# Performance work log

Measured on AMD Instinct MI355X. Metric: run time of the kernel, lower is better.

## Reference

```python
import jax, jax.numpy as jnp
import numpy as np

DIM = 2048
NUM_HEADS = 8
HEAD_DIM = DIM // NUM_HEADS
BATCH = 16384
EPS = 1e-5


def setup_inputs() -> dict:
    key = jax.random.key(0)
    ks = jax.random.split(key, 10)
    s = 1.0 / np.sqrt(DIM)
    inp = {
        "x": jax.random.normal(ks[0], (BATCH, 1, DIM), dtype=jnp.float32),
        "w_q": jax.random.uniform(ks[1], (DIM, DIM), jnp.float32, -s, s),
        "b_q": jax.random.uniform(ks[2], (DIM,), jnp.float32, -s, s),
        "w_k": jax.random.uniform(ks[3], (DIM, DIM), jnp.float32, -s, s),
        "b_k": jax.random.uniform(ks[4], (DIM,), jnp.float32, -s, s),
        "w_v": jax.random.uniform(ks[5], (DIM, DIM), jnp.float32, -s, s),
        "b_v": jax.random.uniform(ks[6], (DIM,), jnp.float32, -s, s),
        "w_o": jax.random.uniform(ks[7], (DIM, DIM), jnp.float32, -s, s),
        "b_o": jax.random.uniform(ks[8], (DIM,), jnp.float32, -s, s),
        "ln_gamma": jnp.ones((DIM,), jnp.float32),
        "ln_beta": jnp.zeros((DIM,), jnp.float32),
    }
    return inp


def _layer_norm(x, gamma, beta):
    mean = jnp.mean(x, axis=-1, keepdims=True)
    var = jnp.mean(jnp.square(x - mean), axis=-1, keepdims=True)
    return (x - mean) * jax.lax.rsqrt(var + EPS) * gamma + beta


def reference(x, w_q, b_q, w_k, b_k, w_v, b_v, w_o, b_o, ln_gamma, ln_beta):
    # x: (B, 1, D). Dropout is identity (eval mode).
    residual = x
    h = _layer_norm(x, ln_gamma, ln_beta)
    q = h @ w_q.T + b_q  # (B, 1, D)
    k = h @ w_k.T + b_k
    v = h @ w_v.T + b_v
    B = x.shape[0]
    # (B, H, 1, hd)
    qh = q.reshape(B, 1, NUM_HEADS, HEAD_DIM).transpose(0, 2, 1, 3)
    kh = k.reshape(B, 1, NUM_HEADS, HEAD_DIM).transpose(0, 2, 1, 3)
    vh = v.reshape(B, 1, NUM_HEADS, HEAD_DIM).transpose(0, 2, 1, 3)
    scale = HEAD_DIM ** -0.5
    # (B, H, 1, 1); with seq_len=1 softmax is trivially 1, but keep the math faithful
    scores = jnp.einsum("bhqd,bhkd->bhqk", qh, kh) * scale
    probs = jax.nn.softmax(scores, axis=-1)
    attn = jnp.einsum("bhqk,bhkd->bhqd", probs, vh)  # (B, H, 1, hd)
    attn = attn.transpose(0, 2, 1, 3).reshape(B, 1, DIM)
    out = attn @ w_o.T + b_o
    out = out + residual
    return out[:, 0, :]  # squeeze seq dim -> (B, D)
```

## Files before the change

### kernel.cpp

```cpp
#include <hip/hip_runtime.h>
#include <hip/hip_bf16.h>
#include <cstdint>

#define D_MODEL 2048
#define N_BATCH 16384

typedef __attribute__((ext_vector_type(8))) __bf16 bf16x8;
typedef __attribute__((ext_vector_type(4))) float f32x4;

__device__ __forceinline__ unsigned short f2bf(float f) {
    unsigned int u = __builtin_bit_cast(unsigned int, f);
    u += 0x7fffu + ((u >> 16) & 1u);
    return (unsigned short)(u >> 16);
}

__global__ __launch_bounds__(256) void ln_kernel(
    const float* __restrict__ x, const float* __restrict__ gamma,
    const float* __restrict__ beta, unsigned short* __restrict__ h)
{
    const int row = blockIdx.x;
    const int t = threadIdx.x;
    const float4* x4 = reinterpret_cast<const float4*>(x + (long)row * D_MODEL);
    float4 a = x4[t];
    float4 b = x4[256 + t];
    float s  = a.x + a.y + a.z + a.w + b.x + b.y + b.z + b.w;
    float ss = a.x*a.x + a.y*a.y + a.z*a.z + a.w*a.w
             + b.x*b.x + b.y*b.y + b.z*b.z + b.w*b.w;
    #pragma unroll
    for (int off = 32; off; off >>= 1) {
        s  += __shfl_xor(s, off);
        ss += __shfl_xor(ss, off);
    }
    __shared__ float red[8];
    const int lane = t & 63, wid = t >> 6;
    if (lane == 0) { red[wid*2] = s; red[wid*2+1] = ss; }
    __syncthreads();
    s  = red[0] + red[2] + red[4] + red[6];
    ss = red[1] + red[3] + red[5] + red[7];
    const float mean = s * (1.0f / D_MODEL);
    const float var  = ss * (1.0f / D_MODEL) - mean * mean;
    const float inv  = rsqrtf(var + 1e-5f);

    const float4* g4  = reinterpret_cast<const float4*>(gamma);
    const float4* be4 = reinterpret_cast<const float4*>(beta);
    ushort4* h4 = reinterpret_cast<ushort4*>(h + (long)row * D_MODEL);
    {
        float4 g = g4[t], be = be4[t];
        ushort4 o;
        o.x = f2bf((a.x - mean) * inv * g.x + be.x);
        o.y = f2bf((a.y - mean) * inv * g.y + be.y);
        o.z = f2bf((a.z - mean) * inv * g.z + be.z);
        o.w = f2bf((a.w - mean) * inv * g.w + be.w);
        h4[t] = o;
    }
    {
        float4 g = g4[256 + t], be = be4[256 + t];
        ushort4 o;
        o.x = f2bf((b.x - mean) * inv * g.x + be.x);
        o.y = f2bf((b.y - mean) * inv * g.y + be.y);
        o.z = f2bf((b.z - mean) * inv * g.z + be.z);
        o.w = f2bf((b.w - mean) * inv * g.w + be.w);
        h4[256 + t] = o;
    }
}

__global__ __launch_bounds__(256) void transpose_f32_to_bf16(
    const float* __restrict__ in, unsigned short* __restrict__ out, int Dm)
{
    __shared__ float tile[32][33];
    const int nb = Dm >> 5;
    const int k0 = (blockIdx.x % nb) * 32;
    const int j0 = (blockIdx.x / nb) * 32;
    const int tx = threadIdx.x & 31, ty0 = threadIdx.x >> 5;
    #pragma unroll
    for (int i = 0; i < 32; i += 8) {
        int j = ty0 + i;
        tile[j][tx] = in[(long)(j0 + j) * Dm + k0 + tx];
    }
    __syncthreads();
    #pragma unroll
    for (int i = 0; i < 32; i += 8) {
        int kk = ty0 + i;
        out[(long)(k0 + kk) * Dm + j0 + tx] = f2bf(tile[tx][kk]);
    }
}

__global__ __launch_bounds__(256) void convert_bf16(
    const float* __restrict__ in, unsigned short* __restrict__ out, long n)
{
    long i = ((long)blockIdx.x * 256 + threadIdx.x) * 8;
    if (i >= n) return;
    const float4* in4 = reinterpret_cast<const float4*>(in + i);
    float4 a = in4[0], b = in4[1];
    union { unsigned short u[8]; uint4 v; } o;
    o.u[0] = f2bf(a.x); o.u[1] = f2bf(a.y); o.u[2] = f2bf(a.z); o.u[3] = f2bf(a.w);
    o.u[4] = f2bf(b.x); o.u[5] = f2bf(b.y); o.u[6] = f2bf(b.z); o.u[7] = f2bf(b.w);
    *reinterpret_cast<uint4*>(out + i) = o.v;
}

__global__ __launch_bounds__(256) void bias_combine(
    const float* __restrict__ w_o, const float* __restrict__ b_v,
    const float* __restrict__ b_o, float* __restrict__ b_c)
{
    const int n = blockIdx.x;
    const int t = threadIdx.x;
    const float4* w4 = reinterpret_cast<const float4*>(w_o + (long)n * D_MODEL);
    const float4* v4 = reinterpret_cast<const float4*>(b_v);
    float4 a = w4[t], b = w4[256 + t], va = v4[t], vb = v4[256 + t];
    float s = a.x*va.x + a.y*va.y + a.z*va.z + a.w*va.w
            + b.x*vb.x + b.y*vb.y + b.z*vb.z + b.w*vb.w;
    #pragma unroll
    for (int off = 32; off; off >>= 1) s += __shfl_xor(s, off);
    __shared__ float red[4];
    const int lane = t & 63, wid = t >> 6;
    if (lane == 0) red[wid] = s;
    __syncthreads();
    if (t == 0) b_c[n] = red[0] + red[1] + red[2] + red[3] + b_o[n];
}

__global__ __launch_bounds__(256, 2) void gemm_bt_128(
    const unsigned short* __restrict__ A, const unsigned short* __restrict__ B,
    unsigned short* __restrict__ C, int M, int N, int K)
{
    const int nBN = N >> 7;
    int wg = blockIdx.x;
    const int nwg = gridDim.x;
    const int cpx = nwg >> 3;
    wg = (wg & 7) * cpx + (wg >> 3);
    const int bm = wg / nBN, bn = wg % nBN;

    const int t = threadIdx.x;
    const int lane = t & 63, wid = t >> 6;
    const int wr = wid >> 1, wc = wid & 1;

    __shared__ __align__(16) unsigned short Alds[128 * 32];
    __shared__ __align__(16) unsigned short Blds[128 * 32];

    f32x4 acc[4][4];
    #pragma unroll
    for (int i = 0; i < 4; i++)
        #pragma unroll
        for (int j = 0; j < 4; j++) acc[i][j] = (f32x4){0.f, 0.f, 0.f, 0.f};

    const long Abase = (long)bm * 128 * K;
    const long Bbase = (long)bn * 128 * K;
    const int ci0 = wid * 64 + lane;
    const int ci1 = 256 + ci0;
    const int r0 = ci0 >> 2, c0 = (ci0 & 3) * 8;
    const int r1 = ci1 >> 2, c1 = (ci1 & 3) * 8;

    const int arow = wr * 64 + (lane & 15);
    const int brow = wc * 64 + (lane & 15);
    const int koff = (lane >> 4) * 8;

    for (int k0 = 0; k0 < K; k0 += 32) {
        __builtin_amdgcn_global_load_lds(
            (const __attribute__((address_space(1))) void*)(A + Abase + (long)r0 * K + k0 + c0),
            (__attribute__((address_space(3))) void*)(Alds + wid * 512), 16, 0, 0);
        __builtin_amdgcn_global_load_lds(
            (const __attribute__((address_space(1))) void*)(A + Abase + (long)r1 * K + k0 + c1),
            (__attribute__((address_space(3))) void*)(Alds + 2048 + wid * 512), 16, 0, 0);
        __builtin_amdgcn_global_load_lds(
            (const __attribute__((address_space(1))) void*)(B + Bbase + (long)r0 * K + k0 + c0),
            (__attribute__((address_space(3))) void*)(Blds + wid * 512), 16, 0, 0);
        __builtin_amdgcn_global_load_lds(
            (const __attribute__((address_space(1))) void*)(B + Bbase + (long)r1 * K + k0 + c1),
            (__attribute__((address_space(3))) void*)(Blds + 2048 + wid * 512), 16, 0, 0);
        __syncthreads();

        bf16x8 af[4], bfr[4];
        #pragma unroll
        for (int m = 0; m < 4; m++)
            af[m] = *reinterpret_cast<const bf16x8*>(&Alds[(arow + m * 16) * 32 + koff]);
        #pragma unroll
        for (int n = 0; n < 4; n++)
            bfr[n] = *reinterpret_cast<const bf16x8*>(&Blds[(brow + n * 16) * 32 + koff]);
        #pragma unroll
        for (int m = 0; m < 4; m++)
            #pragma unroll
            for (int n = 0; n < 4; n++)
                acc[m][n] = __builtin_amdgcn_mfma_f32_16x16x32_bf16(af[m], bfr[n], acc[m][n], 0, 0, 0);
        __syncthreads();
    }

    const int crow0 = bm * 128 + wr * 64 + ((lane >> 4) << 2);
    const int ccol0 = bn * 128 + wc * 64 + (lane & 15);
    #pragma unroll
    for (int m = 0; m < 4; m++)
        #pragma unroll
        for (int j = 0; j < 4; j++) {
            const long r = crow0 + m * 16 + j;
            #pragma unroll
            for (int n = 0; n < 4; n++)
                C[r * N + ccol0 + n * 16] = f2bf(acc[m][n][j]);
        }
}

#define GLL(src, dst) __builtin_amdgcn_global_load_lds( \
    (const __attribute__((address_space(1))) void*)(src), \
    (__attribute__((address_space(3))) void*)(dst), 16, 0, 0)
#define WAITV4() do { asm volatile("s_waitcnt vmcnt(4)" ::: "memory"); \
                      __builtin_amdgcn_sched_barrier(0); } while (0)
#define WAITV0() do { asm volatile("s_waitcnt vmcnt(0)" ::: "memory"); \
                      __builtin_amdgcn_sched_barrier(0); } while (0)

__global__ __launch_bounds__(512, 2) void gemm_bt_8ph(
    const unsigned short* __restrict__ A, const unsigned short* __restrict__ B,
    float* __restrict__ C, const float* __restrict__ bias,
    const float* __restrict__ resid, int M, int N, int K)
{
    __shared__ __align__(16) char ldsb[131072];

    const int nBN = N >> 8;
    int wg = blockIdx.x;
    const int cpx = gridDim.x >> 3;
    wg = (wg & 7) * cpx + (wg >> 3);
    const int bm = wg / nBN, bn = wg % nBN;

    const int t = threadIdx.x;
    const int lane = t & 63, wid = t >> 6;
    const int wr = wid >> 2;
    const int wc = wid & 3;

    const long Kl = K;
    const int tr = t >> 3;
    const int c8 = ((t & 7) ^ (tr & 7)) * 8;
    const unsigned short* As = A + (long)(bm * 256 + tr) * Kl + c8;
    const unsigned short* Bs = B + (long)(bn * 256 + tr) * Kl + c8;

#define ST_A(buf, half, kcol) do { \
    const unsigned short* s_ = As + (half) * 128 * Kl + (kcol); \
    char* d_ = ldsb + (buf) * 65536 + (half) * 16384 + t * 16; \
    GLL(s_, d_); GLL(s_ + 64 * Kl, d_ + 8192); } while (0)
#define ST_B(buf, half, kcol) do { \
    const unsigned short* s_ = Bs + (half) * 128 * Kl + (kcol); \
    char* d_ = ldsb + (buf) * 65536 + 32768 + (half) * 16384 + t * 16; \
    GLL(s_, d_); GLL(s_ + 64 * Kl, d_ + 8192); } while (0)

    const int l15 = lane & 15, l4 = lane >> 4;
    const int swz0 = ((l4)     ^ (l15 & 7)) << 4;
    const int swz1 = ((4 + l4) ^ (l15 & 7)) << 4;
    const int aOff = wr * 16384 + l15 * 128;
    const int bOff = 32768 + (wc >> 1) * 16384 + ((wc & 1) * 64 + l15) * 128;

#define LDV(off) (*reinterpret_cast<const bf16x8*>(ldsb + (off)))
#define RD_A(buf, mh) do { _Pragma("unroll") for (int mi = 0; mi < 4; ++mi) { \
    af[mi][0] = LDV((buf) * 65536 + aOff + ((mh) * 4 + mi) * 2048 + swz0); \
    af[mi][1] = LDV((buf) * 65536 + aOff + ((mh) * 4 + mi) * 2048 + swz1); } } while (0)
#define RD_B0(buf) do { _Pragma("unroll") for (int nj = 0; nj < 2; ++nj) { \
    b0[nj][0] = LDV((buf) * 65536 + bOff + nj * 2048 + swz0); \
    b0[nj][1] = LDV((buf) * 65536 + bOff + nj * 2048 + swz1); } } while (0)
#define RD_B1(buf) do { _Pragma("unroll") for (int nj = 0; nj < 2; ++nj) { \
    b1[nj][0] = LDV((buf) * 65536 + bOff + (2 + nj) * 2048 + swz0); \
    b1[nj][1] = LDV((buf) * 65536 + bOff + (2 + nj) * 2048 + swz1); } } while (0)

#define MMQ(mh, nh, BQ) do { \
    __builtin_amdgcn_s_barrier(); \
    asm volatile("s_waitcnt lgkmcnt(0)" ::: "memory"); \
    __builtin_amdgcn_sched_barrier(0); \
    __builtin_amdgcn_s_setprio(1); \
    _Pragma("unroll") for (int mi = 0; mi < 4; ++mi) \
    _Pragma("unroll") for (int nj = 0; nj < 2; ++nj) \
    _Pragma("unroll") for (int kk = 0; kk < 2; ++kk) \
        acc[(mh) * 4 + mi][(nh) * 2 + nj] = __builtin_amdgcn_mfma_f32_16x16x32_bf16( \
            af[mi][kk], BQ[nj][kk], acc[(mh) * 4 + mi][(nh) * 2 + nj], 0, 0, 0); \
    __builtin_amdgcn_s_setprio(0); } while (0)
#define ENDP() __builtin_amdgcn_s_barrier()

    bf16x8 af[4][2], b0[2][2], b1[2][2];
    f32x4 acc[8][4];
    #pragma unroll
    for (int i = 0; i < 8; i++)
        #pragma unroll
        for (int j = 0; j < 4; j++) acc[i][j] = (f32x4){0.f, 0.f, 0.f, 0.f};

    const int NI = K >> 7;

    ST_A(0, 0, 0); ST_A(0, 1, 0); ST_B(0, 0, 0); ST_B(0, 1, 0);
    ST_B(1, 0, 64); ST_B(1, 1, 64);
    WAITV4();
    __builtin_amdgcn_s_barrier();

    for (int i = 0; i < NI; ++i) {
        const int kcA1 = (i << 7) + 64;
        const int kcN0 = (i << 7) + 128;
        const int kcN1 = (i << 7) + 192;
        const bool more = (i + 1 < NI);

        RD_A(0, 0); RD_B0(0);
        ST_A(1, 0, kcA1);
        MMQ(0, 0, b0); ENDP();
        RD_B1(0);
        ST_A(1, 1, kcA1);
        MMQ(0, 1, b1); ENDP();
        RD_A(0, 1);
        if (more) ST_B(0, 0, kcN0);
        MMQ(1, 0, b0); ENDP();
        if (more) ST_B(0, 1, kcN0);
        MMQ(1, 1, b1);
        if (more) { WAITV4(); } else { WAITV0(); }
        ENDP();
        RD_A(1, 0); RD_B0(1);
        if (more) ST_A(0, 0, kcN0);
        MMQ(0, 0, b0); ENDP();
        RD_B1(1);
        if (more) ST_A(0, 1, kcN0);
        MMQ(0, 1, b1); ENDP();
        RD_A(1, 1);
        if (more) ST_B(1, 0, kcN1);
        MMQ(1, 0, b0); ENDP();
        if (more) ST_B(1, 1, kcN1);
        MMQ(1, 1, b1);
        if (more) { WAITV4(); }
        ENDP();
    }
#undef ST_A
#undef ST_B
#undef RD_A
#undef RD_B0
#undef RD_B1
#undef MMQ
#undef ENDP
#undef LDV

    const int crow0 = bm * 256 + wr * 128 + l4 * 4;
    const int ccol0 = bn * 256 + wc * 64 + l15;
    #pragma unroll
    for (int m = 0; m < 8; m++)
        #pragma unroll
        for (int j = 0; j < 4; j++) {
            const long r = crow0 + m * 16 + j;
            float* crow = C + r * N;
            const float* rrow = resid + r * N;
            #pragma unroll
            for (int n = 0; n < 4; n++) {
                const int col = ccol0 + n * 16;
                crow[col] = acc[m][n][j] + bias[col] + rrow[col];
            }
        }
}

extern "C" void kernel_launch(void* const* d_in, const int* in_sizes, int n_in,
                              void* d_out, int out_size, void* d_ws, size_t ws_size,
                              hipStream_t stream) {
    const float* x     = (const float*)d_in[0];
    const float* w_v   = (const float*)d_in[5];
    const float* b_v   = (const float*)d_in[6];
    const float* w_o   = (const float*)d_in[7];
    const float* b_o   = (const float*)d_in[8];
    const float* gamma = (const float*)d_in[9];
    const float* beta  = (const float*)d_in[10];
    float* out = (float*)d_out;

    char* ws = (char*)d_ws;
    unsigned short* h   = (unsigned short*)(ws);
    unsigned short* wvT = (unsigned short*)(ws + 67108864L);
    unsigned short* woB = (unsigned short*)(ws + 67108864L + 8388608L);
    unsigned short* Wc  = (unsigned short*)(ws + 67108864L + 2 * 8388608L);
    float*          b_c = (float*)(ws + 67108864L + 3 * 8388608L);

    ln_kernel<<<N_BATCH, 256, 0, stream>>>(x, gamma, beta, h);
    transpose_f32_to_bf16<<<(D_MODEL / 32) * (D_MODEL / 32), 256, 0, stream>>>(w_v, wvT, D_MODEL);
    convert_bf16<<<(D_MODEL * (long)D_MODEL) / (256 * 8), 256, 0, stream>>>(w_o, woB, (long)D_MODEL * D_MODEL);
    bias_combine<<<D_MODEL, 256, 0, stream>>>(w_o, b_v, b_o, b_c);
    gemm_bt_128<<<(D_MODEL / 128) * (D_MODEL / 128), 256, 0, stream>>>(
        woB, wvT, Wc, D_MODEL, D_MODEL, D_MODEL);
    gemm_bt_8ph<<<(N_BATCH / 256) * (D_MODEL / 256), 512, 0, stream>>>(
        h, Wc, out, b_c, x, N_BATCH, D_MODEL, D_MODEL);
}
```

Baseline: 242.7 us.

## Merge prep kernels and co-schedule weight GEMM with LayerNorm; reorder main GEMM loads

Result: faster. 232.7 us (-4.1%).

```diff
diff --git a/kernel.cpp b/kernel.cpp
--- a/kernel.cpp
+++ b/kernel.cpp
@@ -14,186 +14,178 @@
     return (unsigned short)(u >> 16);
 }
 
-__global__ __launch_bounds__(256) void ln_kernel(
+__global__ __launch_bounds__(256) void prep_kernel(
+    const float* __restrict__ w_v, const float* __restrict__ w_o,
+    const float* __restrict__ b_v, const float* __restrict__ b_o,
+    unsigned short* __restrict__ wvT, unsigned short* __restrict__ woB,
+    float* __restrict__ b_c)
+{
+    __shared__ float tile[32][33];
+    const int b = blockIdx.x;
+    const int t = threadIdx.x;
+    if (b < 4096) {
+        const int nb = 64;
+        const int k0 = (b % nb) * 32;
+        const int j0 = (b / nb) * 32;
+        const int tx = t & 31, ty0 = t >> 5;
+        #pragma unroll
+        for (int i = 0; i < 32; i += 8) {
+            int j = ty0 + i;
+            tile[j][tx] = w_v[(long)(j0 + j) * D_MODEL + k0 + tx];
+        }
+        __syncthreads();
+        #pragma unroll
+        for (int i = 0; i < 32; i += 8) {
+            int kk = ty0 + i;
+            wvT[(long)(k0 + kk) * D_MODEL + j0 + tx] = f2bf(tile[tx][kk]);
+        }
+    } else if (b < 6144) {
+        long i = ((long)(b - 4096) * 256 + t) * 8;
+        const float4* in4 = reinterpret_cast<const float4*>(w_o + i);
+        float4 a = in4[0], bb = in4[1];
+        union { unsigned short u[8]; uint4 v; } o;
+        o.u[0] = f2bf(a.x); o.u[1] = f2bf(a.y); o.u[2] = f2bf(a.z); o.u[3] = f2bf(a.w);
+        o.u[4] = f2bf(bb.x); o.u[5] = f2bf(bb.y); o.u[6] = f2bf(bb.z); o.u[7] = f2bf(bb.w);
+        *reinterpret_cast<uint4*>(woB + i) = o.v;
+    } else {
+        const int n = b - 6144;
+        const float4* w4 = reinterpret_cast<const float4*>(w_o + (long)n * D_MODEL);
+        const float4* v4 = reinterpret_cast<const float4*>(b_v);
+        float4 a = w4[t], bb = w4[256 + t], va = v4[t], vb = v4[256 + t];
+        float s = a.x*va.x + a.y*va.y + a.z*va.z + a.w*va.w
+                + bb.x*vb.x + bb.y*vb.y + bb.z*vb.z + bb.w*vb.w;
+        #pragma unroll
+        for (int off = 32; off; off >>= 1) s += __shfl_xor(s, off);
+        float* red = &tile[0][0];
+        const int lane = t & 63, wid = t >> 6;
+        if (lane == 0) red[wid] = s;
+        __syncthreads();
+        if (t == 0) b_c[n] = red[0] + red[1] + red[2] + red[3] + b_o[n];
+    }
+}
+
+__global__ __launch_bounds__(256) void lnwc_kernel(
+    const unsigned short* __restrict__ A, const unsigned short* __restrict__ B,
+    unsigned short* __restrict__ C,
     const float* __restrict__ x, const float* __restrict__ gamma,
     const float* __restrict__ beta, unsigned short* __restrict__ h)
 {
-    const int row = blockIdx.x;
-    const int t = threadIdx.x;
-    const float4* x4 = reinterpret_cast<const float4*>(x + (long)row * D_MODEL);
-    float4 a = x4[t];
-    float4 b = x4[256 + t];
-    float s  = a.x + a.y + a.z + a.w + b.x + b.y + b.z + b.w;
-    float ss = a.x*a.x + a.y*a.y + a.z*a.z + a.w*a.w
-             + b.x*b.x + b.y*b.y + b.z*b.z + b.w*b.w;
-    #pragma unroll
-    for (int off = 32; off; off >>= 1) {
-        s  += __shfl_xor(s, off);
-        ss += __shfl_xor(ss, off);
-    }
-    __shared__ float red[8];
-    const int lane = t & 63, wid = t >> 6;
-    if (lane == 0) { red[wid*2] = s; red[wid*2+1] = ss; }
-    __syncthreads();
-    s  = red[0] + red[2] + red[4] + red[6];
-    ss = red[1] + red[3] + red[5] + red[7];
-    const float mean = s * (1.0f / D_MODEL);
-    const float var  = ss * (1.0f / D_MODEL) - mean * mean;
-    const float inv  = rsqrtf(var + 1e-5f);
-
-    const float4* g4  = reinterpret_cast<const float4*>(gamma);
-    const float4* be4 = reinterpret_cast<const float4*>(beta);
-    ushort4* h4 = reinterpret_cast<ushort4*>(h + (long)row * D_MODEL);
-    {
-        float4 g = g4[t], be = be4[t];
-        ushort4 o;
-        o.x = f2bf((a.x - mean) * inv * g.x + be.x);
-        o.y = f2bf((a.y - mean) * inv * g.y + be.y);
-        o.z = f2bf((a.z - mean) * inv * g.z + be.z);
-        o.w = f2bf((a.w - mean) * inv * g.w + be.w);
-        h4[t] = o;
-    }
-    {
-        float4 g = g4[256 + t], be = be4[256 + t];
-        ushort4 o;
-        o.x = f2bf((b.x - mean) * inv * g.x + be.x);
-        o.y = f2bf((b.y - mean) * inv * g.y + be.y);
-        o.z = f2bf((b.z - mean) * inv * g.z + be.z);
-        o.w = f2bf((b.w - mean) * inv * g.w + be.w);
-        h4[256 + t] = o;
-    }
-}
-
-__global__ __launch_bounds__(256) void transpose_f32_to_bf16(
-    const float* __restrict__ in, unsigned short* __restrict__ out, int Dm)
-{
-    __shared__ float tile[32][33];
-    const int nb = Dm >> 5;
-    const int k0 = (blockIdx.x % nb) * 32;
-    const int j0 = (blockIdx.x / nb) * 32;
-    const int tx = threadIdx.x & 31, ty0 = threadIdx.x >> 5;
-    #pragma unroll
-    for (int i = 0; i < 32; i += 8) {
-        int j = ty0 + i;
-        tile[j][tx] = in[(long)(j0 + j) * Dm + k0 + tx];
-    }
-    __syncthreads();
-    #pragma unroll
-    for (int i = 0; i < 32; i += 8) {
-        int kk = ty0 + i;
-        out[(long)(k0 + kk) * Dm + j0 + tx] = f2bf(tile[tx][kk]);
-    }
-}
-
-__global__ __launch_bounds__(256) void convert_bf16(
-    const float* __restrict__ in, unsigned short* __restrict__ out, long n)
-{
-    long i = ((long)blockIdx.x * 256 + threadIdx.x) * 8;
-    if (i >= n) return;
-    const float4* in4 = reinterpret_cast<const float4*>(in + i);
-    float4 a = in4[0], b = in4[1];
-    union { unsigned short u[8]; uint4 v; } o;
-    o.u[0] = f2bf(a.x); o.u[1] = f2bf(a.y); o.u[2] = f2bf(a.z); o.u[3] = f2bf(a.w);
-    o.u[4] = f2bf(b.x); o.u[5] = f2bf(b.y); o.u[6] = f2bf(b.z); o.u[7] = f2bf(b.w);
-    *reinterpret_cast<uint4*>(out + i) = o.v;
-}
-
-__global__ __launch_bounds__(256) void bias_combine(
-    const float* __restrict__ w_o, const float* __restrict__ b_v,
-    const float* __restrict__ b_o, float* __restrict__ b_c)
-{
-    const int n = blockIdx.x;
-    const int t = threadIdx.x;
-    const float4* w4 = reinterpret_cast<const float4*>(w_o + (long)n * D_MODEL);
-    const float4* v4 = reinterpret_cast<const float4*>(b_v);
-    float4 a = w4[t], b = w4[256 + t], va = v4[t], vb = v4[256 + t];
-    float s = a.x*va.x + a.y*va.y + a.z*va.z + a.w*va.w
-            + b.x*vb.x + b.y*vb.y + b.z*vb.z + b.w*vb.w;
-    #pragma unroll
-    for (int off = 32; off; off >>= 1) s += __shfl_xor(s, off);
-    __shared__ float red[4];
-    const int lane = t & 63, wid = t >> 6;
-    if (lane == 0) red[wid] = s;
-    __syncthreads();
-    if (t == 0) b_c[n] = red[0] + red[1] + red[2] + red[3] + b_o[n];
-}
-
-__global__ __launch_bounds__(256, 2) void gemm_bt_128(
-    const unsigned short* __restrict__ A, const unsigned short* __restrict__ B,
-    unsigned short* __restrict__ C, int M, int N, int K)
-{
-    const int nBN = N >> 7;
-    int wg = blockIdx.x;
-    const int nwg = gridDim.x;
-    const int cpx = nwg >> 3;
-    wg = (wg & 7) * cpx + (wg >> 3);
-    const int bm = wg / nBN, bn = wg % nBN;
-
-    const int t = threadIdx.x;
-    const int lane = t & 63, wid = t >> 6;
-    const int wr = wid >> 1, wc = wid & 1;
-
     __shared__ __align__(16) unsigned short Alds[128 * 32];
     __shared__ __align__(16) unsigned short Blds[128 * 32];
-
-    f32x4 acc[4][4];
-    #pragma unroll
-    for (int i = 0; i < 4; i++)
-        #pragma unroll
-        for (int j = 0; j < 4; j++) acc[i][j] = (f32x4){0.f, 0.f, 0.f, 0.f};
-
-    const long Abase = (long)bm * 128 * K;
-    const long Bbase = (long)bn * 128 * K;
-    const int ci0 = wid * 64 + lane;
-    const int ci1 = 256 + ci0;
-    const int r0 = ci0 >> 2, c0 = (ci0 & 3) * 8;
-    const int r1 = ci1 >> 2, c1 = (ci1 & 3) * 8;
-
-    const int arow = wr * 64 + (lane & 15);
-    const int brow = wc * 64 + (lane & 15);
-    const int koff = (lane >> 4) * 8;
-
-    for (int k0 = 0; k0 < K; k0 += 32) {
-        __builtin_amdgcn_global_load_lds(
-            (const __attribute__((address_space(1))) void*)(A + Abase + (long)r0 * K + k0 + c0),
-            (__attribute__((address_space(3))) void*)(Alds + wid * 512), 16, 0, 0);
-        __builtin_amdgcn_global_load_lds(
-            (const __attribute__((address_space(1))) void*)(A + Abase + (long)r1 * K + k0 + c1),
-            (__attribute__((address_space(3))) void*)(Alds + 2048 + wid * 512), 16, 0, 0);
-        __builtin_amdgcn_global_load_lds(
-            (const __attribute__((address_space(1))) void*)(B + Bbase + (long)r0 * K + k0 + c0),
-            (__attribute__((address_space(3))) void*)(Blds + wid * 512), 16, 0, 0);
-        __builtin_amdgcn_global_load_lds(
-            (const __attribute__((address_space(1))) void*)(B + Bbase + (long)r1 * K + k0 + c1),
-            (__attribute__((address_space(3))) void*)(Blds + 2048 + wid * 512), 16, 0, 0);
+    const int t = threadIdx.x;
+
+    if (blockIdx.x < 256) {
+        const int K = D_MODEL, N = D_MODEL;
+        int wg = blockIdx.x;
+        wg = (wg & 7) * 32 + (wg >> 3);
+        const int bm = wg >> 4, bn = wg & 15;
+
+        const int lane = t & 63, wid = t >> 6;
+        const int wr = wid >> 1, wc = wid & 1;
+
+        f32x4 acc[4][4];
+        #pragma unroll
+        for (int i = 0; i < 4; i++)
+            #pragma unroll
+            for (int j = 0; j < 4; j++) acc[i][j] = (f32x4){0.f, 0.f, 0.f, 0.f};
+
+        const long Abase = (long)bm * 128 * K;
+        const long Bbase = (long)bn * 128 * K;
+        const int ci0 = wid * 64 + lane;
+        const int ci1 = 256 + ci0;
+        const int r0 = ci0 >> 2, c0 = (ci0 & 3) * 8;
+        const int r1 = ci1 >> 2, c1 = (ci1 & 3) * 8;
+
+        const int arow = wr * 64 + (lane & 15);
+        const int brow = wc * 64 + (lane & 15);
+        const int koff = (lane >> 4) * 8;
+
+        for (int k0 = 0; k0 < K; k0 += 32) {
+            __builtin_amdgcn_global_load_lds(
+                (const __attribute__((address_space(1))) void*)(A + Abase + (long)r0 * K + k0 + c0),
+                (__attribute__((address_space(3))) void*)(Alds + wid * 512), 16, 0, 0);
+            __builtin_amdgcn_global_load_lds(
+                (const __attribute__((address_space(1))) void*)(A + Abase + (long)r1 * K + k0 + c1),
+                (__attribute__((address_space(3))) void*)(Alds + 2048 + wid * 512), 16, 0, 0);
+            __builtin_amdgcn_global_load_lds(
+                (const __attribute__((address_space(1))) void*)(B + Bbase + (long)r0 * K + k0 + c0),
+                (__attribute__((address_space(3))) void*)(Blds + wid * 512), 16, 0, 0);
+            __builtin_amdgcn_global_load_lds(
+                (const __attribute__((address_space(1))) void*)(B + Bbase + (long)r1 * K + k0 + c1),
+                (__attribute__((address_space(3))) void*)(Blds + 2048 + wid * 512), 16, 0, 0);
+            __syncthreads();
+
+            bf16x8 af[4], bfr[4];
+            #pragma unroll
+            for (int m = 0; m < 4; m++)
+                af[m] = *reinterpret_cast<const bf16x8*>(&Alds[(arow + m * 16) * 32 + koff]);
+            #pragma unroll
+            for (int n = 0; n < 4; n++)
+                bfr[n] = *reinterpret_cast<const bf16x8*>(&Blds[(brow + n * 16) * 32 + koff]);
+            #pragma unroll
+            for (int m = 0; m < 4; m++)
+                #pragma unroll
+                for (int n = 0; n < 4; n++)
+                    acc[m][n] = __builtin_amdgcn_mfma_f32_16x16x32_bf16(af[m], bfr[n], acc[m][n], 0, 0, 0);
+            __syncthreads();
+        }
+
+        const int crow0 = bm * 128 + wr * 64 + ((lane >> 4) << 2);
+        const int ccol0 = bn * 128 + wc * 64 + (lane & 15);
+        #pragma unroll
+        for (int m = 0; m < 4; m++)
+            #pragma unroll
+            for (int j = 0; j < 4; j++) {
+                const long r = crow0 + m * 16 + j;
+                #pragma unroll
+                for (int n = 0; n < 4; n++)
+                    C[r * N + ccol0 + n * 16] = f2bf(acc[m][n][j]);
+            }
+    } else {
+        const int row = blockIdx.x - 256;
+        const float4* x4 = reinterpret_cast<const float4*>(x + (long)row * D_MODEL);
+        float4 a = x4[t];
+        float4 b = x4[256 + t];
+        float s  = a.x + a.y + a.z + a.w + b.x + b.y + b.z + b.w;
+        float ss = a.x*a.x + a.y*a.y + a.z*a.z + a.w*a.w
+                 + b.x*b.x + b.y*b.y + b.z*b.z + b.w*b.w;
+        #pragma unroll
+        for (int off = 32; off; off >>= 1) {
+            s  += __shfl_xor(s, off);
+            ss += __shfl_xor(ss, off);
+        }
+        float* red = reinterpret_cast<float*>(Alds);
+        const int lane = t & 63, wid = t >> 6;
+        if (lane == 0) { red[wid*2] = s; red[wid*2+1] = ss; }
         __syncthreads();
-
-        bf16x8 af[4], bfr[4];
-        #pragma unroll
-        for (int m = 0; m < 4; m++)
-            af[m] = *reinterpret_cast<const bf16x8*>(&Alds[(arow + m * 16) * 32 + koff]);
-        #pragma unroll
-        for (int n = 0; n < 4; n++)
-            bfr[n] = *reinterpret_cast<const bf16x8*>(&Blds[(brow + n * 16) * 32 + koff]);
-        #pragma unroll
-        for (int m = 0; m < 4; m++)
-            #pragma unroll
-            for (int n = 0; n < 4; n++)
-                acc[m][n] = __builtin_amdgcn_mfma_f32_16x16x32_bf16(af[m], bfr[n], acc[m][n], 0, 0, 0);
-        __syncthreads();
+        s  = red[0] + red[2] + red[4] + red[6];
+        ss = red[1] + red[3] + red[5] + red[7];
+        const float mean = s * (1.0f / D_MODEL);
+        const float var  = ss * (1.0f / D_MODEL) - mean * mean;
+        const float inv  = rsqrtf(var + 1e-5f);
+
+        const float4* g4  = reinterpret_cast<const float4*>(gamma);
+        const float4* be4 = reinterpret_cast<const float4*>(beta);
+        ushort4* h4 = reinterpret_cast<ushort4*>(h + (long)row * D_MODEL);
+        {
+            float4 g = g4[t], be = be4[t];
+            ushort4 o;
+            o.x = f2bf((a.x - mean) * inv * g.x + be.x);
+            o.y = f2bf((a.y - mean) * inv * g.y + be.y);
+            o.z = f2bf((a.z - mean) * inv * g.z + be.z);
+            o.w = f2bf((a.w - mean) * inv * g.w + be.w);
+            h4[t] = o;
+        }
+        {
+            float4 g = g4[256 + t], be = be4[256 + t];
+            ushort4 o;
+            o.x = f2bf((b.x - mean) * inv * g.x + be.x);
+            o.y = f2bf((b.y - mean) * inv * g.y + be.y);
+            o.z = f2bf((b.z - mean) * inv * g.z + be.z);
+            o.w = f2bf((b.w - mean) * inv * g.w + be.w);
+            h4[256 + t] = o;
+        }
     }
-
-    const int crow0 = bm * 128 + wr * 64 + ((lane >> 4) << 2);
-    const int ccol0 = bn * 128 + wc * 64 + (lane & 15);
-    #pragma unroll
-    for (int m = 0; m < 4; m++)
-        #pragma unroll
-        for (int j = 0; j < 4; j++) {
-            const long r = crow0 + m * 16 + j;
-            #pragma unroll
-            for (int n = 0; n < 4; n++)
-                C[r * N + ccol0 + n * 16] = f2bf(acc[m][n][j]);
-        }
 }
 
 #define GLL(src, dst) __builtin_amdgcn_global_load_lds( \
@@ -259,9 +251,9 @@
     asm volatile("s_waitcnt lgkmcnt(0)" ::: "memory"); \
     __builtin_amdgcn_sched_barrier(0); \
     __builtin_amdgcn_s_setprio(1); \
+    _Pragma("unroll") for (int kk = 0; kk < 2; ++kk) \
     _Pragma("unroll") for (int mi = 0; mi < 4; ++mi) \
     _Pragma("unroll") for (int nj = 0; nj < 2; ++nj) \
-    _Pragma("unroll") for (int kk = 0; kk < 2; ++kk) \
         acc[(mh) * 4 + mi][(nh) * 2 + nj] = __builtin_amdgcn_mfma_f32_16x16x32_bf16( \
             af[mi][kk], BQ[nj][kk], acc[(mh) * 4 + mi][(nh) * 2 + nj], 0, 0, 0); \
     __builtin_amdgcn_s_setprio(0); } while (0)
@@ -277,7 +269,7 @@
     const int NI = K >> 7;
 
     ST_A(0, 0, 0); ST_A(0, 1, 0); ST_B(0, 0, 0); ST_B(0, 1, 0);
-    ST_B(1, 0, 64); ST_B(1, 1, 64);
+    ST_B(1, 0, 64); ST_A(1, 0, 64);
     WAITV4();
     __builtin_amdgcn_s_barrier();
 
@@ -288,28 +280,28 @@
         const bool more = (i + 1 < NI);
 
         RD_A(0, 0); RD_B0(0);
-        ST_A(1, 0, kcA1);
+        ST_A(1, 1, kcA1);
         MMQ(0, 0, b0); ENDP();
         RD_B1(0);
-        ST_A(1, 1, kcA1);
+        ST_B(1, 1, kcA1);
         MMQ(0, 1, b1); ENDP();
         RD_A(0, 1);
         if (more) ST_B(0, 0, kcN0);
         MMQ(1, 0, b0); ENDP();
-        if (more) ST_B(0, 1, kcN0);
+        if (more) ST_A(0, 0, kcN0);
         MMQ(1, 1, b1);
         if (more) { WAITV4(); } else { WAITV0(); }
         ENDP();
         RD_A(1, 0); RD_B0(1);
-        if (more) ST_A(0, 0, kcN0);
+        if (more) ST_A(0, 1, kcN0);
         MMQ(0, 0, b0); ENDP();
         RD_B1(1);
-        if (more) ST_A(0, 1, kcN0);
+        if (more) ST_B(0, 1, kcN0);
         MMQ(0, 1, b1); ENDP();
         RD_A(1, 1);
         if (more) ST_B(1, 0, kcN1);
         MMQ(1, 0, b0); ENDP();
-        if (more) ST_B(1, 1, kcN1);
+        if (more) ST_A(1, 0, kcN1);
         MMQ(1, 1, b1);
         if (more) { WAITV4(); }
         ENDP();
@@ -359,12 +351,8 @@
     unsigned short* Wc  = (unsigned short*)(ws + 67108864L + 2 * 8388608L);
     float*          b_c = (float*)(ws + 67108864L + 3 * 8388608L);
 
-    ln_kernel<<<N_BATCH, 256, 0, stream>>>(x, gamma, beta, h);
-    transpose_f32_to_bf16<<<(D_MODEL / 32) * (D_MODEL / 32), 256, 0, stream>>>(w_v, wvT, D_MODEL);
-    convert_bf16<<<(D_MODEL * (long)D_MODEL) / (256 * 8), 256, 0, stream>>>(w_o, woB, (long)D_MODEL * D_MODEL);
-    bias_combine<<<D_MODEL, 256, 0, stream>>>(w_o, b_v, b_o, b_c);
-    gemm_bt_128<<<(D_MODEL / 128) * (D_MODEL / 128), 256, 0, stream>>>(
-        woB, wvT, Wc, D_MODEL, D_MODEL, D_MODEL);
+    prep_kernel<<<8192, 256, 0, stream>>>(w_v, w_o, b_v, b_o, wvT, woB, b_c);
+    lnwc_kernel<<<256 + N_BATCH, 256, 0, stream>>>(woB, wvT, Wc, x, gamma, beta, h);
     gemm_bt_8ph<<<(N_BATCH / 256) * (D_MODEL / 256), 512, 0, stream>>>(
         h, Wc, out, b_c, x, N_BATCH, D_MODEL, D_MODEL);
 }
```
